# Optimization experiments

Measured on AMD Instinct MI355X. Metric: run time of the kernel, lower is better.

Reference implementation:

```python
import jax, jax.numpy as jnp
import numpy as np

N, D, K = 65536, 128, 2048  # n_cells, latent_dim, nmb_prototypes


def setup_inputs() -> dict:
    key = jax.random.key(0)
    k1, k2, k3, k4, k5 = jax.random.split(key, 5)
    x = jax.random.normal(k1, (N, D), dtype=jnp.float32)
    # nn.Linear default init scale ~ 1/sqrt(fan_in)
    W_proto = jax.random.normal(k2, (K, D), dtype=jnp.float32) * (1.0 / np.sqrt(D))
    recon_loss = jax.random.uniform(k3, (), dtype=jnp.float32)
    kl_loss = jax.random.uniform(k4, (), dtype=jnp.float32)
    mmd_loss = jax.random.uniform(k5, (), dtype=jnp.float32)
    return {"x": x, "W_proto": W_proto, "recon_loss": recon_loss,
            "kl_loss": kl_loss, "mmd_loss": mmd_loss}


def _pairwise_dist(z, w):
    # torch.cdist(z, w, p=2) via the matmul expansion (use_mm_for_euclid_dist)
    zz = jnp.sum(z * z, axis=1, keepdims=True)       # [N, 1]
    ww = jnp.sum(w * w, axis=1, keepdims=True).T     # [1, K]
    sq = zz + ww - 2.0 * (z @ w.T)                   # [N, K]
    return jnp.sqrt(jnp.maximum(sq, 0.0))


def reference(x, W_proto, recon_loss, kl_loss, mmd_loss):
    # cvae loss combination (compute_cvae_loss, calc_alpha_coeff = 0.5)
    cvae_loss = recon_loss + 0.5 * kl_loss + mmd_loss
    # F.normalize(x, dim=1, p=2): x / max(||x||_2, eps)
    nrm = jnp.maximum(jnp.linalg.norm(x, axis=1, keepdims=True), 1e-12)
    z = x / nrm                                      # [N, D]
    # self.prototypes(x): Linear without bias
    logits = z @ W_proto.T                           # [N, K]
    # prototype_decoding_loss: one NxK distance matrix reduced two ways
    dist = _pairwise_dist(z, W_proto)                # [N, K]
    propagation = jnp.mean(jnp.min(dist, axis=1))    # nearest prototype per cell
    emb_similarity = jnp.mean(jnp.min(dist, axis=0))  # nearest cell per prototype
    # forward returns (x, x, prototypes(x), cvae_loss, (prop, emb_sim)); x duplicated
    return (z, logits, cvae_loss, propagation, emb_similarity)
```

## Files before the change

kernel.cpp:

```cpp
#include <hip/hip_runtime.h>
#include <hip/hip_bf16.h>
#include <math.h>

#define N_CELLS 65536
#define D_DIM   128
#define K_PROTO 2048

typedef __attribute__((ext_vector_type(8))) short bf16x8;
typedef __attribute__((ext_vector_type(4))) float f32x4;

__device__ __forceinline__ unsigned int f2bf(float f) {
  unsigned int u = __float_as_uint(f);
  return ((u + 0x7FFFu + ((u >> 16) & 1u)) >> 16) & 0xFFFFu;
}

__global__ __launch_bounds__(256) void normalize_k(
    const float* __restrict__ x, float* __restrict__ z,
    unsigned int* __restrict__ zb) {
  int tid = threadIdx.x;
  int sub = tid & 31;
  int row = blockIdx.x * 8 + (tid >> 5);
  const f32x4* xr = (const f32x4*)(x + (size_t)row * D_DIM);
  f32x4 v = xr[sub];
  float s = v.x * v.x + v.y * v.y + v.z * v.z + v.w * v.w;
  #pragma unroll
  for (int off = 1; off < 32; off <<= 1) s += __shfl_xor(s, off, 64);
  float inv = 1.0f / fmaxf(sqrtf(s), 1e-12f);
  f32x4 zv = v * inv;
  __builtin_nontemporal_store(zv, (f32x4*)(z + (size_t)row * D_DIM) + sub);
  unsigned int lo = (f2bf(zv.y) << 16) | f2bf(zv.x);
  unsigned int h2 = (f2bf(zv.w) << 16) | f2bf(zv.z);
  unsigned long long pk = ((unsigned long long)h2 << 32) | lo;
  *((unsigned long long*)(zb + (size_t)row * (D_DIM / 2)) + sub) = pk;
}

__global__ __launch_bounds__(256) void wprep_k(
    const float* __restrict__ W, unsigned int* __restrict__ wb,
    float* __restrict__ ww,
    const float* __restrict__ recon, const float* __restrict__ kl,
    const float* __restrict__ mmd, float* __restrict__ scal) {
  if (blockIdx.x == 0 && threadIdx.x == 0) {
    scal[0] = recon[0] + 0.5f * kl[0] + mmd[0];
  }
  int tid = threadIdx.x;
  int sub = tid & 31;
  int row = blockIdx.x * 8 + (tid >> 5);
  const f32x4* wr = (const f32x4*)(W + (size_t)row * D_DIM);
  f32x4 v = wr[sub];
  float s = v.x * v.x + v.y * v.y + v.z * v.z + v.w * v.w;
  #pragma unroll
  for (int off = 1; off < 32; off <<= 1) s += __shfl_xor(s, off, 64);
  if (sub == 0) ww[row] = s;
  unsigned int lo = (f2bf(v.y) << 16) | f2bf(v.x);
  unsigned int h2 = (f2bf(v.w) << 16) | f2bf(v.z);
  unsigned long long pk = ((unsigned long long)h2 << 32) | lo;
  *((unsigned long long*)(wb + (size_t)row * (D_DIM / 2)) + sub) = pk;
}

__global__ __launch_bounds__(256) void gemm_k(
    const unsigned short* __restrict__ zb, const unsigned short* __restrict__ wb,
    const float* __restrict__ ww, float* __restrict__ logits,
    float* __restrict__ rowmin_part, float* __restrict__ colmax_part) {
  __shared__ float cs[128 * 128];
  __shared__ float rmin[2][128];
  __shared__ float cmx[2][128];

  int bid = blockIdx.x;
  int swz = (bid & 7) * 1024 + (bid >> 3);
  int nt  = swz & 15;
  int mt  = swz >> 4;

  int tid  = threadIdx.x;
  int lane = tid & 63;
  int wid  = tid >> 6;
  int wrow = (wid >> 1) * 64;
  int wcol = (wid & 1) * 64;
  int l15  = lane & 15;
  int hi   = lane >> 4;

  const char* Abase = (const char*)zb + ((size_t)(mt * 128 + wrow + l15) * 256 + hi * 16);
  const char* Bbase = (const char*)wb + ((size_t)(nt * 128 + wcol + l15) * 256 + hi * 16);

  f32x4 acc[4][4];
  #pragma unroll
  for (int i = 0; i < 4; ++i)
    #pragma unroll
    for (int j = 0; j < 4; ++j)
      acc[i][j] = f32x4{0.f, 0.f, 0.f, 0.f};

  #pragma unroll
  for (int kk = 0; kk < 4; ++kk) {
    bf16x8 a[4], b[4];
    #pragma unroll
    for (int i = 0; i < 4; ++i) a[i] = *(const bf16x8*)(Abase + i * 4096 + kk * 64);
    #pragma unroll
    for (int j = 0; j < 4; ++j) b[j] = *(const bf16x8*)(Bbase + j * 4096 + kk * 64);
    #pragma unroll
    for (int i = 0; i < 4; ++i)
      #pragma unroll
      for (int j = 0; j < 4; ++j)
        acc[i][j] = __builtin_amdgcn_mfma_f32_16x16x32_bf16(b[j], a[i], acc[i][j], 0, 0, 0);
  }

  int gcolbase = nt * 128 + wcol;
  f32x4 wwj[4];
  #pragma unroll
  for (int j = 0; j < 4; ++j)
    wwj[j] = *(const f32x4*)(ww + gcolbase + j * 16 + hi * 4);

  #pragma unroll
  for (int i = 0; i < 4; ++i) {
    float vmin = 1e30f;
    #pragma unroll
    for (int j = 0; j < 4; ++j)
      #pragma unroll
      for (int r = 0; r < 4; ++r) vmin = fminf(vmin, wwj[j][r] - 2.0f * acc[i][j][r]);
    vmin = fminf(vmin, __shfl_xor(vmin, 16, 64));
    vmin = fminf(vmin, __shfl_xor(vmin, 32, 64));
    if (hi == 0) rmin[wid & 1][wrow + i * 16 + l15] = vmin;
  }

  #pragma unroll
  for (int j = 0; j < 4; ++j) {
    f32x4 m = acc[0][j];
    #pragma unroll
    for (int i = 1; i < 4; ++i)
      #pragma unroll
      for (int r = 0; r < 4; ++r) m[r] = fmaxf(m[r], acc[i][j][r]);
    #pragma unroll
    for (int s2 = 1; s2 < 16; s2 <<= 1)
      #pragma unroll
      for (int r = 0; r < 4; ++r) m[r] = fmaxf(m[r], __shfl_xor(m[r], s2, 64));
    if (l15 == 0)
      *(f32x4*)&cmx[wid >> 1][wcol + j * 16 + hi * 4] = m;
  }

  #pragma unroll
  for (int i = 0; i < 4; ++i) {
    int row = wrow + i * 16 + l15;
    #pragma unroll
    for (int j = 0; j < 4; ++j) {
      int g  = (wcol >> 2) + j * 4 + hi;
      int pg = g ^ ((row & 7) << 2);
      *(f32x4*)((char*)cs + row * 512 + pg * 16) = acc[i][j];
    }
  }
  __syncthreads();

  if (tid < 128) {
    rowmin_part[(size_t)nt * N_CELLS + mt * 128 + tid] =
        fminf(rmin[0][tid], rmin[1][tid]);
  } else {
    int c = tid - 128;
    colmax_part[(size_t)mt * K_PROTO + nt * 128 + c] =
        fmaxf(cmx[0][c], cmx[1][c]);
  }

  {
    int l31  = lane & 31;
    int rsub = lane >> 5;
    #pragma unroll
    for (int it = 0; it < 16; ++it) {
      int row = it * 8 + wid * 2 + rsub;
      int pg  = l31 ^ ((row & 7) << 2);
      f32x4 c = *(const f32x4*)((const char*)cs + row * 512 + pg * 16);
      size_t grow = (size_t)mt * 128 + row;
      __builtin_nontemporal_store(c, (f32x4*)(logits + grow * K_PROTO + nt * 128 + l31 * 4));
    }
  }
}

__global__ __launch_bounds__(1024) void prop1_k(
    const float* __restrict__ rowmin_part, float* __restrict__ prop_part) {
  __shared__ float sbuf[16];
  int slot = blockIdx.x * 1024 + threadIdx.x;
  f32x4 v = *(const f32x4*)(rowmin_part + (size_t)slot * 4);
  #pragma unroll
  for (int p = 1; p < 16; ++p) {
    f32x4 u = *(const f32x4*)(rowmin_part + (size_t)p * N_CELLS + (size_t)slot * 4);
    #pragma unroll
    for (int r = 0; r < 4; ++r) v[r] = fminf(v[r], u[r]);
  }
  float s = 0.f;
  #pragma unroll
  for (int r = 0; r < 4; ++r) s += sqrtf(fmaxf(1.0f + v[r], 0.0f));
  #pragma unroll
  for (int off = 1; off < 64; off <<= 1) s += __shfl_xor(s, off, 64);
  int wv = threadIdx.x >> 6, lane = threadIdx.x & 63;
  if (lane == 0) sbuf[wv] = s;
  __syncthreads();
  if (threadIdx.x == 0) {
    float t = 0.f;
    #pragma unroll
    for (int w = 0; w < 16; ++w) t += sbuf[w];
    prop_part[blockIdx.x] = t;
  }
}

__global__ __launch_bounds__(1024) void emb1_k(
    const float* __restrict__ colmax_part, const float* __restrict__ ww,
    float* __restrict__ emb_part) {
  __shared__ float buf[8][128];
  __shared__ float sbuf[2];
  int t   = threadIdx.x;
  int col = blockIdx.x * 128 + (t & 127);
  int seg = t >> 7;
  float m = -1e30f;
  for (int k = 0; k < 64; ++k)
    m = fmaxf(m, colmax_part[(size_t)(seg * 64 + k) * K_PROTO + col]);
  buf[seg][t & 127] = m;
  __syncthreads();
  if (t < 128) {
    float tot = buf[0][t];
    #pragma unroll
    for (int s2 = 1; s2 < 8; ++s2) tot = fmaxf(tot, buf[s2][t]);
    float val = sqrtf(fmaxf(1.0f + ww[col] - 2.0f * tot, 0.0f));
    #pragma unroll
    for (int off = 1; off < 64; off <<= 1) val += __shfl_xor(val, off, 64);
    if ((t & 63) == 0) sbuf[t >> 6] = val;
  }
  __syncthreads();
  if (t == 0) emb_part[blockIdx.x] = sbuf[0] + sbuf[1];
}

__global__ __launch_bounds__(64) void final_k(
    const float* __restrict__ prop_part, const float* __restrict__ emb_part,
    float* __restrict__ scal) {
  if (threadIdx.x == 0) {
    float p = 0.f, e = 0.f;
    #pragma unroll
    for (int i = 0; i < 16; ++i) { p += prop_part[i]; e += emb_part[i]; }
    scal[1] = p * (1.0f / N_CELLS);
    scal[2] = e * (1.0f / K_PROTO);
  }
}

extern "C" void kernel_launch(void* const* d_in, const int* in_sizes, int n_in,
                              void* d_out, int out_size, void* d_ws, size_t ws_size,
                              hipStream_t stream) {
  const float* x     = (const float*)d_in[0];
  const float* W     = (const float*)d_in[1];
  const float* recon = (const float*)d_in[2];
  const float* kl    = (const float*)d_in[3];
  const float* mmd   = (const float*)d_in[4];

  float* out    = (float*)d_out;
  float* z      = out;
  float* logits = out + (size_t)N_CELLS * D_DIM;
  float* scal   = logits + (size_t)N_CELLS * K_PROTO;

  char* ws = (char*)d_ws;
  unsigned int* zb = (unsigned int*)ws;
  size_t off = (size_t)N_CELLS * D_DIM * 2;
  unsigned int* wb = (unsigned int*)(ws + off);
  off += (size_t)K_PROTO * D_DIM * 2;
  float* ww = (float*)(ws + off);
  off += (size_t)K_PROTO * 4;
  float* rowmin_part = (float*)(ws + off);
  off += (size_t)16 * N_CELLS * 4;
  float* colmax_part = (float*)(ws + off);
  off += (size_t)512 * K_PROTO * 4;
  float* prop_part = (float*)(ws + off);
  off += 16 * 4;
  float* emb_part = (float*)(ws + off);

  normalize_k<<<N_CELLS / 8, 256, 0, stream>>>(x, z, zb);
  wprep_k<<<K_PROTO / 8, 256, 0, stream>>>(W, wb, ww, recon, kl, mmd, scal);
  gemm_k<<<(N_CELLS / 128) * (K_PROTO / 128), 256, 0, stream>>>(
      (const unsigned short*)zb, (const unsigned short*)wb, ww, logits,
      rowmin_part, colmax_part);
  prop1_k<<<16, 1024, 0, stream>>>(rowmin_part, prop_part);
  emb1_k<<<16, 1024, 0, stream>>>(colmax_part, ww, emb_part);
  final_k<<<1, 64, 0, stream>>>(prop_part, emb_part, scal);
}
```

Measured before the change: 191.9 us.

## Loop each GEMM block over four column tiles reusing register-held A fragments

Each GEMM workgroup now handles one 128-row tile across four consecutive 128-column prototype tiles. It loads the A (z) fragments into registers once, and row minima accumulate in registers across the four tiles. This cuts the grid from 8192 to 2048 blocks, removes repeated A loads, and shrinks the row-min partial buffer from 16 to 4 slices, so the propagation reduction reads less. In exchange it raises register pressure (A fragments plus accumulators), adds extra barriers per tile, and lowers parallelism, which may hurt occupancy.

New measurement: 219.8 us. 14.5% more time.

```diff
diff --git a/kernel.cpp b/kernel.cpp
--- a/kernel.cpp
+++ b/kernel.cpp
@@ -66,9 +66,8 @@
   __shared__ float cmx[2][128];
 
   int bid = blockIdx.x;
-  int swz = (bid & 7) * 1024 + (bid >> 3);
-  int nt  = swz & 15;
-  int mt  = swz >> 4;
+  int mt  = (bid & 7) * 64 + (bid >> 5);
+  int ntg = (bid >> 3) & 3;
 
   int tid  = threadIdx.x;
   int lane = tid & 63;
@@ -79,94 +78,116 @@
   int hi   = lane >> 4;
 
   const char* Abase = (const char*)zb + ((size_t)(mt * 128 + wrow + l15) * 256 + hi * 16);
-  const char* Bbase = (const char*)wb + ((size_t)(nt * 128 + wcol + l15) * 256 + hi * 16);
-
-  f32x4 acc[4][4];
+  bf16x8 afr[4][4];
   #pragma unroll
   for (int i = 0; i < 4; ++i)
     #pragma unroll
+    for (int kk = 0; kk < 4; ++kk)
+      afr[i][kk] = *(const bf16x8*)(Abase + i * 4096 + kk * 64);
+
+  float vrm[4];
+  #pragma unroll
+  for (int i = 0; i < 4; ++i) vrm[i] = 1e30f;
+
+  #pragma unroll
+  for (int t = 0; t < 4; ++t) {
+    int nt = ntg * 4 + t;
+    const char* Bbase = (const char*)wb + ((size_t)(nt * 128 + wcol + l15) * 256 + hi * 16);
+
+    f32x4 acc[4][4];
+    #pragma unroll
+    for (int i = 0; i < 4; ++i)
+      #pragma unroll
+      for (int j = 0; j < 4; ++j)
+        acc[i][j] = f32x4{0.f, 0.f, 0.f, 0.f};
+
+    #pragma unroll
+    for (int kk = 0; kk < 4; ++kk) {
+      bf16x8 b[4];
+      #pragma unroll
+      for (int j = 0; j < 4; ++j) b[j] = *(const bf16x8*)(Bbase + j * 4096 + kk * 64);
+      #pragma unroll
+      for (int i = 0; i < 4; ++i)
+        #pragma unroll
+        for (int j = 0; j < 4; ++j)
+          acc[i][j] = __builtin_amdgcn_mfma_f32_16x16x32_bf16(b[j], afr[i][kk], acc[i][j], 0, 0, 0);
+    }
+
+    int gcolbase = nt * 128 + wcol;
+    f32x4 wwj[4];
+    #pragma unroll
     for (int j = 0; j < 4; ++j)
-      acc[i][j] = f32x4{0.f, 0.f, 0.f, 0.f};
-
-  #pragma unroll
-  for (int kk = 0; kk < 4; ++kk) {
-    bf16x8 a[4], b[4];
-    #pragma unroll
-    for (int i = 0; i < 4; ++i) a[i] = *(const bf16x8*)(Abase + i * 4096 + kk * 64);
-    #pragma unroll
-    for (int j = 0; j < 4; ++j) b[j] = *(const bf16x8*)(Bbase + j * 4096 + kk * 64);
-    #pragma unroll
-    for (int i = 0; i < 4; ++i)
+      wwj[j] = *(const f32x4*)(ww + gcolbase + j * 16 + hi * 4);
+
+    #pragma unroll
+    for (int i = 0; i < 4; ++i) {
+      float vmin = 1e30f;
       #pragma unroll
       for (int j = 0; j < 4; ++j)
-        acc[i][j] = __builtin_amdgcn_mfma_f32_16x16x32_bf16(b[j], a[i], acc[i][j], 0, 0, 0);
-  }
-
-  int gcolbase = nt * 128 + wcol;
-  f32x4 wwj[4];
-  #pragma unroll
-  for (int j = 0; j < 4; ++j)
-    wwj[j] = *(const f32x4*)(ww + gcolbase + j * 16 + hi * 4);
-
-  #pragma unroll
-  for (int i = 0; i < 4; ++i) {
-    float vmin = 1e30f;
-    #pragma unroll
-    for (int j = 0; j < 4; ++j)
-      #pragma unroll
-      for (int r = 0; r < 4; ++r) vmin = fminf(vmin, wwj[j][r] - 2.0f * acc[i][j][r]);
-    vmin = fminf(vmin, __shfl_xor(vmin, 16, 64));
-    vmin = fminf(vmin, __shfl_xor(vmin, 32, 64));
-    if (hi == 0) rmin[wid & 1][wrow + i * 16 + l15] = vmin;
-  }
-
-  #pragma unroll
-  for (int j = 0; j < 4; ++j) {
-    f32x4 m = acc[0][j];
-    #pragma unroll
-    for (int i = 1; i < 4; ++i)
-      #pragma unroll
-      for (int r = 0; r < 4; ++r) m[r] = fmaxf(m[r], acc[i][j][r]);
-    #pragma unroll
-    for (int s2 = 1; s2 < 16; s2 <<= 1)
-      #pragma unroll
-      for (int r = 0; r < 4; ++r) m[r] = fmaxf(m[r], __shfl_xor(m[r], s2, 64));
-    if (l15 == 0)
-      *(f32x4*)&cmx[wid >> 1][wcol + j * 16 + hi * 4] = m;
-  }
-
-  #pragma unroll
-  for (int i = 0; i < 4; ++i) {
-    int row = wrow + i * 16 + l15;
+        #pragma unroll
+        for (int r = 0; r < 4; ++r) vmin = fminf(vmin, wwj[j][r] - 2.0f * acc[i][j][r]);
+      vmin = fminf(vmin, __shfl_xor(vmin, 16, 64));
+      vmin = fminf(vmin, __shfl_xor(vmin, 32, 64));
+      vrm[i] = fminf(vrm[i], vmin);
+    }
+
+    __syncthreads();
+
     #pragma unroll
     for (int j = 0; j < 4; ++j) {
-      int g  = (wcol >> 2) + j * 4 + hi;
-      int pg = g ^ ((row & 7) << 2);
-      *(f32x4*)((char*)cs + row * 512 + pg * 16) = acc[i][j];
-    }
-  }
-  __syncthreads();
-
+      f32x4 m = acc[0][j];
+      #pragma unroll
+      for (int i = 1; i < 4; ++i)
+        #pragma unroll
+        for (int r = 0; r < 4; ++r) m[r] = fmaxf(m[r], acc[i][j][r]);
+      #pragma unroll
+      for (int s2 = 1; s2 < 16; s2 <<= 1)
+        #pragma unroll
+        for (int r = 0; r < 4; ++r) m[r] = fmaxf(m[r], __shfl_xor(m[r], s2, 64));
+      if (l15 == 0)
+        *(f32x4*)&cmx[wid >> 1][wcol + j * 16 + hi * 4] = m;
+    }
+
+    #pragma unroll
+    for (int i = 0; i < 4; ++i) {
+      int row = wrow + i * 16 + l15;
+      #pragma unroll
+      for (int j = 0; j < 4; ++j) {
+        int g  = (wcol >> 2) + j * 4 + hi;
+        int pg = g ^ ((row & 7) << 2);
+        *(f32x4*)((char*)cs + row * 512 + pg * 16) = acc[i][j];
+      }
+    }
+    __syncthreads();
+
+    if (tid >= 128) {
+      int c = tid - 128;
+      colmax_part[(size_t)mt * K_PROTO + nt * 128 + c] =
+          fmaxf(cmx[0][c], cmx[1][c]);
+    }
+
+    {
+      int l31  = lane & 31;
+      int rsub = lane >> 5;
+      #pragma unroll
+      for (int it = 0; it < 16; ++it) {
+        int row = it * 8 + wid * 2 + rsub;
+        int pg  = l31 ^ ((row & 7) << 2);
+        f32x4 c = *(const f32x4*)((const char*)cs + row * 512 + pg * 16);
+        size_t grow = (size_t)mt * 128 + row;
+        __builtin_nontemporal_store(c, (f32x4*)(logits + grow * K_PROTO + nt * 128 + l31 * 4));
+      }
+    }
+  }
+
+  if (hi == 0) {
+    #pragma unroll
+    for (int i = 0; i < 4; ++i) rmin[wid & 1][wrow + i * 16 + l15] = vrm[i];
+  }
+  __syncthreads();
   if (tid < 128) {
-    rowmin_part[(size_t)nt * N_CELLS + mt * 128 + tid] =
+    rowmin_part[(size_t)ntg * N_CELLS + mt * 128 + tid] =
         fminf(rmin[0][tid], rmin[1][tid]);
-  } else {
-    int c = tid - 128;
-    colmax_part[(size_t)mt * K_PROTO + nt * 128 + c] =
-        fmaxf(cmx[0][c], cmx[1][c]);
-  }
-
-  {
-    int l31  = lane & 31;
-    int rsub = lane >> 5;
-    #pragma unroll
-    for (int it = 0; it < 16; ++it) {
-      int row = it * 8 + wid * 2 + rsub;
-      int pg  = l31 ^ ((row & 7) << 2);
-      f32x4 c = *(const f32x4*)((const char*)cs + row * 512 + pg * 16);
-      size_t grow = (size_t)mt * 128 + row;
-      __builtin_nontemporal_store(c, (f32x4*)(logits + grow * K_PROTO + nt * 128 + l31 * 4));
-    }
   }
 }
 
@@ -176,7 +197,7 @@
   int slot = blockIdx.x * 1024 + threadIdx.x;
   f32x4 v = *(const f32x4*)(rowmin_part + (size_t)slot * 4);
   #pragma unroll
-  for (int p = 1; p < 16; ++p) {
+  for (int p = 1; p < 4; ++p) {
     f32x4 u = *(const f32x4*)(rowmin_part + (size_t)p * N_CELLS + (size_t)slot * 4);
     #pragma unroll
     for (int r = 0; r < 4; ++r) v[r] = fminf(v[r], u[r]);
@@ -257,7 +278,7 @@
   float* ww = (float*)(ws + off);
   off += (size_t)K_PROTO * 4;
   float* rowmin_part = (float*)(ws + off);
-  off += (size_t)16 * N_CELLS * 4;
+  off += (size_t)4 * N_CELLS * 4;
   float* colmax_part = (float*)(ws + off);
   off += (size_t)512 * K_PROTO * 4;
   float* prop_part = (float*)(ws + off);
@@ -266,7 +287,7 @@
 
   normalize_k<<<N_CELLS / 8, 256, 0, stream>>>(x, z, zb);
   wprep_k<<<K_PROTO / 8, 256, 0, stream>>>(W, wb, ww, recon, kl, mmd, scal);
-  gemm_k<<<(N_CELLS / 128) * (K_PROTO / 128), 256, 0, stream>>>(
+  gemm_k<<<2048, 256, 0, stream>>>(
       (const unsigned short*)zb, (const unsigned short*)wb, ww, logits,
       rowmin_part, colmax_part);
   prop1_k<<<16, 1024, 0, stream>>>(rowmin_part, prop_part);
```

## Retile GEMM to 32x512 blocks with smaller LDS staging and direct colmax writes

Applied to the files above, without the earlier changes.

The GEMM tile changes from 128x128 to 32 rows by 512 columns, with each wave owning a 32x128 strip. The logits epilogue is staged through a 32 KB LDS buffer in two 16-row halves instead of one 64 KB buffer. The aim is to raise occupancy (launch bounds of 3 blocks) and cut LDS pressure. Column-max partials now go straight to global memory, so the colmax partial array grows fourfold and the emb reduction must read more data. Rowmin partials shrink from 16 to 4 slices, and operand reuse per block changes because A is reused less and B more.

Result: slower. 259.6 us (+35.2%).

```diff
diff --git a/kernel.cpp b/kernel.cpp
--- a/kernel.cpp
+++ b/kernel.cpp
@@ -12,6 +12,14 @@
 __device__ __forceinline__ unsigned int f2bf(float f) {
   unsigned int u = __float_as_uint(f);
   return ((u + 0x7FFFu + ((u >> 16) & 1u)) >> 16) & 0xFFFFu;
+}
+
+__device__ __forceinline__ void lds_barrier() {
+  __builtin_amdgcn_sched_barrier(0);
+  asm volatile("s_waitcnt lgkmcnt(0)" ::: "memory");
+  __builtin_amdgcn_sched_barrier(0);
+  __builtin_amdgcn_s_barrier();
+  __builtin_amdgcn_sched_barrier(0);
 }
 
 __global__ __launch_bounds__(256) void normalize_k(
@@ -57,116 +65,129 @@
   *((unsigned long long*)(wb + (size_t)row * (D_DIM / 2)) + sub) = pk;
 }
 
-__global__ __launch_bounds__(256) void gemm_k(
+__global__ __launch_bounds__(256, 3) void gemm_k(
     const unsigned short* __restrict__ zb, const unsigned short* __restrict__ wb,
     const float* __restrict__ ww, float* __restrict__ logits,
     float* __restrict__ rowmin_part, float* __restrict__ colmax_part) {
-  __shared__ float cs[128 * 128];
-  __shared__ float rmin[2][128];
-  __shared__ float cmx[2][128];
+  __shared__ float cs[16 * 512];
+  __shared__ float rmin[4][32];
 
   int bid = blockIdx.x;
-  int swz = (bid & 7) * 1024 + (bid >> 3);
-  int nt  = swz & 15;
-  int mt  = swz >> 4;
+  int ntg = (bid >> 3) & 3;
+  int mt  = (bid & 7) * 256 + (bid >> 5);
 
   int tid  = threadIdx.x;
   int lane = tid & 63;
-  int wid  = tid >> 6;
-  int wrow = (wid >> 1) * 64;
-  int wcol = (wid & 1) * 64;
+  int wq   = tid >> 6;
   int l15  = lane & 15;
   int hi   = lane >> 4;
 
-  const char* Abase = (const char*)zb + ((size_t)(mt * 128 + wrow + l15) * 256 + hi * 16);
-  const char* Bbase = (const char*)wb + ((size_t)(nt * 128 + wcol + l15) * 256 + hi * 16);
-
-  f32x4 acc[4][4];
-  #pragma unroll
-  for (int i = 0; i < 4; ++i)
-    #pragma unroll
-    for (int j = 0; j < 4; ++j)
+  int colbase = ntg * 512 + wq * 128;
+
+  const char* Abase = (const char*)zb + ((size_t)(mt * 32 + l15) * 256 + hi * 16);
+  const char* Bbase = (const char*)wb + ((size_t)(colbase + l15) * 256 + hi * 16);
+
+  f32x4 acc[2][8];
+  #pragma unroll
+  for (int i = 0; i < 2; ++i)
+    #pragma unroll
+    for (int j = 0; j < 8; ++j)
       acc[i][j] = f32x4{0.f, 0.f, 0.f, 0.f};
 
   #pragma unroll
   for (int kk = 0; kk < 4; ++kk) {
-    bf16x8 a[4], b[4];
-    #pragma unroll
-    for (int i = 0; i < 4; ++i) a[i] = *(const bf16x8*)(Abase + i * 4096 + kk * 64);
-    #pragma unroll
-    for (int j = 0; j < 4; ++j) b[j] = *(const bf16x8*)(Bbase + j * 4096 + kk * 64);
-    #pragma unroll
-    for (int i = 0; i < 4; ++i)
+    bf16x8 a[2], b[8];
+    #pragma unroll
+    for (int i = 0; i < 2; ++i) a[i] = *(const bf16x8*)(Abase + i * 4096 + kk * 64);
+    #pragma unroll
+    for (int j = 0; j < 8; ++j) b[j] = *(const bf16x8*)(Bbase + j * 4096 + kk * 64);
+    #pragma unroll
+    for (int i = 0; i < 2; ++i)
       #pragma unroll
-      for (int j = 0; j < 4; ++j)
+      for (int j = 0; j < 8; ++j)
         acc[i][j] = __builtin_amdgcn_mfma_f32_16x16x32_bf16(b[j], a[i], acc[i][j], 0, 0, 0);
   }
 
-  int gcolbase = nt * 128 + wcol;
-  f32x4 wwj[4];
-  #pragma unroll
-  for (int j = 0; j < 4; ++j)
-    wwj[j] = *(const f32x4*)(ww + gcolbase + j * 16 + hi * 4);
-
-  #pragma unroll
-  for (int i = 0; i < 4; ++i) {
+  f32x4 wwj[8];
+  #pragma unroll
+  for (int j = 0; j < 8; ++j)
+    wwj[j] = *(const f32x4*)(ww + colbase + j * 16 + hi * 4);
+
+  #pragma unroll
+  for (int i = 0; i < 2; ++i) {
     float vmin = 1e30f;
     #pragma unroll
-    for (int j = 0; j < 4; ++j)
+    for (int j = 0; j < 8; ++j)
       #pragma unroll
       for (int r = 0; r < 4; ++r) vmin = fminf(vmin, wwj[j][r] - 2.0f * acc[i][j][r]);
     vmin = fminf(vmin, __shfl_xor(vmin, 16, 64));
     vmin = fminf(vmin, __shfl_xor(vmin, 32, 64));
-    if (hi == 0) rmin[wid & 1][wrow + i * 16 + l15] = vmin;
-  }
-
-  #pragma unroll
-  for (int j = 0; j < 4; ++j) {
+    if (hi == 0) rmin[wq][i * 16 + l15] = vmin;
+  }
+
+  #pragma unroll
+  for (int j = 0; j < 8; ++j) {
     f32x4 m = acc[0][j];
     #pragma unroll
-    for (int i = 1; i < 4; ++i)
-      #pragma unroll
-      for (int r = 0; r < 4; ++r) m[r] = fmaxf(m[r], acc[i][j][r]);
+    for (int r = 0; r < 4; ++r) m[r] = fmaxf(m[r], acc[1][j][r]);
     #pragma unroll
     for (int s2 = 1; s2 < 16; s2 <<= 1)
       #pragma unroll
       for (int r = 0; r < 4; ++r) m[r] = fmaxf(m[r], __shfl_xor(m[r], s2, 64));
     if (l15 == 0)
-      *(f32x4*)&cmx[wid >> 1][wcol + j * 16 + hi * 4] = m;
-  }
-
-  #pragma unroll
-  for (int i = 0; i < 4; ++i) {
-    int row = wrow + i * 16 + l15;
-    #pragma unroll
-    for (int j = 0; j < 4; ++j) {
-      int g  = (wcol >> 2) + j * 4 + hi;
-      int pg = g ^ ((row & 7) << 2);
-      *(f32x4*)((char*)cs + row * 512 + pg * 16) = acc[i][j];
-    }
-  }
-  __syncthreads();
-
-  if (tid < 128) {
-    rowmin_part[(size_t)nt * N_CELLS + mt * 128 + tid] =
-        fminf(rmin[0][tid], rmin[1][tid]);
-  } else {
-    int c = tid - 128;
-    colmax_part[(size_t)mt * K_PROTO + nt * 128 + c] =
-        fmaxf(cmx[0][c], cmx[1][c]);
-  }
-
-  {
-    int l31  = lane & 31;
-    int rsub = lane >> 5;
-    #pragma unroll
-    for (int it = 0; it < 16; ++it) {
-      int row = it * 8 + wid * 2 + rsub;
-      int pg  = l31 ^ ((row & 7) << 2);
-      f32x4 c = *(const f32x4*)((const char*)cs + row * 512 + pg * 16);
-      size_t grow = (size_t)mt * 128 + row;
-      __builtin_nontemporal_store(c, (f32x4*)(logits + grow * K_PROTO + nt * 128 + l31 * 4));
-    }
+      *(f32x4*)(colmax_part + (size_t)mt * K_PROTO + colbase + j * 16 + hi * 4) = m;
+  }
+
+  #pragma unroll
+  for (int j = 0; j < 8; ++j) {
+    int row = l15;
+    int g   = wq * 32 + j * 4 + hi;
+    int pg  = g ^ (row & 7);
+    *(f32x4*)((char*)cs + row * 2048 + pg * 16) = acc[0][j];
+  }
+  lds_barrier();
+
+  if (tid < 32) {
+    float v = fminf(fminf(rmin[0][tid], rmin[1][tid]),
+                    fminf(rmin[2][tid], rmin[3][tid]));
+    rowmin_part[(size_t)ntg * N_CELLS + mt * 32 + tid] = v;
+  }
+
+  #pragma unroll
+  for (int it = 0; it < 8; ++it) {
+    int chunk = it * 4 + wq;
+    int row   = chunk >> 1;
+    int h     = chunk & 1;
+    int g     = h * 64 + lane;
+    int pg    = g ^ (row & 7);
+    f32x4 c = *(const f32x4*)((const char*)cs + row * 2048 + pg * 16);
+    size_t grow = (size_t)mt * 32 + row;
+    __builtin_nontemporal_store(c,
+        (f32x4*)(logits + grow * K_PROTO + ntg * 512 + h * 256 + lane * 4));
+  }
+
+  lds_barrier();
+
+  #pragma unroll
+  for (int j = 0; j < 8; ++j) {
+    int row = l15;
+    int g   = wq * 32 + j * 4 + hi;
+    int pg  = g ^ (row & 7);
+    *(f32x4*)((char*)cs + row * 2048 + pg * 16) = acc[1][j];
+  }
+  lds_barrier();
+
+  #pragma unroll
+  for (int it = 0; it < 8; ++it) {
+    int chunk = it * 4 + wq;
+    int row   = chunk >> 1;
+    int h     = chunk & 1;
+    int g     = h * 64 + lane;
+    int pg    = g ^ (row & 7);
+    f32x4 c = *(const f32x4*)((const char*)cs + row * 2048 + pg * 16);
+    size_t grow = (size_t)mt * 32 + 16 + row;
+    __builtin_nontemporal_store(c,
+        (f32x4*)(logits + grow * K_PROTO + ntg * 512 + h * 256 + lane * 4));
   }
 }
 
@@ -176,7 +197,7 @@
   int slot = blockIdx.x * 1024 + threadIdx.x;
   f32x4 v = *(const f32x4*)(rowmin_part + (size_t)slot * 4);
   #pragma unroll
-  for (int p = 1; p < 16; ++p) {
+  for (int p = 1; p < 4; ++p) {
     f32x4 u = *(const f32x4*)(rowmin_part + (size_t)p * N_CELLS + (size_t)slot * 4);
     #pragma unroll
     for (int r = 0; r < 4; ++r) v[r] = fminf(v[r], u[r]);
@@ -206,8 +227,8 @@
   int col = blockIdx.x * 128 + (t & 127);
   int seg = t >> 7;
   float m = -1e30f;
-  for (int k = 0; k < 64; ++k)
-    m = fmaxf(m, colmax_part[(size_t)(seg * 64 + k) * K_PROTO + col]);
+  for (int k = 0; k < 256; ++k)
+    m = fmaxf(m, colmax_part[(size_t)(seg * 256 + k) * K_PROTO + col]);
   buf[seg][t & 127] = m;
   __syncthreads();
   if (t < 128) {
@@ -257,16 +278,16 @@
   float* ww = (float*)(ws + off);
   off += (size_t)K_PROTO * 4;
   float* rowmin_part = (float*)(ws + off);
-  off += (size_t)16 * N_CELLS * 4;
+  off += (size_t)4 * N_CELLS * 4;
   float* colmax_part = (float*)(ws + off);
-  off += (size_t)512 * K_PROTO * 4;
+  off += (size_t)2048 * K_PROTO * 4;
   float* prop_part = (float*)(ws + off);
   off += 16 * 4;
   float* emb_part = (float*)(ws + off);
 
   normalize_k<<<N_CELLS / 8, 256, 0, stream>>>(x, z, zb);
   wprep_k<<<K_PROTO / 8, 256, 0, stream>>>(W, wb, ww, recon, kl, mmd, scal);
-  gemm_k<<<(N_CELLS / 128) * (K_PROTO / 128), 256, 0, stream>>>(
+  gemm_k<<<8192, 256, 0, stream>>>(
       (const unsigned short*)zb, (const unsigned short*)wb, ww, logits,
       rowmin_part, colmax_part);
   prop1_k<<<16, 1024, 0, stream>>>(rowmin_part, prop_part);
```
